# Kernel tuning notes

Measured on AMD Instinct MI355X. Metric: run time of the kernel, lower is better.

Reference implementation:

```python
import jax, jax.numpy as jnp
import numpy as np

NEG_SLOPE = 0.2
EPS = 1e-16

def gatv2(x, edge_index, edge_attr, Wl, bl, We, att, bias):
    """PyG GATv2Conv, heads=1, share_weights=True, with edge_dim."""
    N = x.shape[0]
    h = x @ Wl + bl                      # [N, out] shared lin_l == lin_r
    src, dst = edge_index[0], edge_index[1]
    hj = h[src]                          # source (message) features [E, out]
    hi = h[dst]                          # target features [E, out]
    e = jax.nn.leaky_relu(hi + hj + edge_attr @ We, NEG_SLOPE)  # [E, out]
    score = e @ att                      # [E]
    # segment softmax over edges grouped by destination node
    smax = jax.ops.segment_max(score, dst, num_segments=N)
    ex = jnp.exp(score - smax[dst])
    denom = jax.ops.segment_sum(ex, dst, num_segments=N)
    alpha = ex / (denom[dst] + EPS)      # [E]
    out = jax.ops.segment_sum(hj * alpha[:, None], dst, num_segments=N)
    return out + bias


def setup_inputs() -> dict:
    key = jax.random.key(0)
    N, E = 50000, 800000
    D_IN, D_LAT, D_EDGE, N_ACT = 128, 128, 16, 32
    ks = jax.random.split(key, 16)
    s = 0.05
    inp = {
        "x": jax.random.normal(ks[0], (N, D_IN), jnp.float32),
        "edge_index": jax.random.randint(ks[1], (2, E), 0, N, jnp.int32),
        "edge_attr": jax.random.normal(ks[2], (E, D_EDGE), jnp.float32),
        # gnn_layer: D_IN -> D_LAT
        "Wl1": jax.random.normal(ks[3], (D_IN, D_LAT), jnp.float32) * s,
        "bl1": jnp.zeros((D_LAT,), jnp.float32),
        "We1": jax.random.normal(ks[4], (D_EDGE, D_LAT), jnp.float32) * s,
        "att1": jax.random.normal(ks[5], (D_LAT,), jnp.float32) * s,
        "bias1": jnp.zeros((D_LAT,), jnp.float32),
        # node_layer: D_LAT -> 1
        "Wl2": jax.random.normal(ks[6], (D_LAT, 1), jnp.float32) * s,
        "bl2": jnp.zeros((1,), jnp.float32),
        "We2": jax.random.normal(ks[7], (D_EDGE, 1), jnp.float32) * s,
        "att2": jax.random.normal(ks[8], (1,), jnp.float32) * s,
        "bias2": jnp.zeros((1,), jnp.float32),
        # action_layer: D_LAT -> N_ACT
        "Wl3": jax.random.normal(ks[9], (D_LAT, N_ACT), jnp.float32) * s,
        "bl3": jnp.zeros((N_ACT,), jnp.float32),
        "We3": jax.random.normal(ks[10], (D_EDGE, N_ACT), jnp.float32) * s,
        "att3": jax.random.normal(ks[11], (N_ACT,), jnp.float32) * s,
        "bias3": jnp.zeros((N_ACT,), jnp.float32),
    }
    return inp


def reference(x, edge_index, edge_attr,
              Wl1, bl1, We1, att1, bias1,
              Wl2, bl2, We2, att2, bias2,
              Wl3, bl3, We3, att3, bias3):
    latent = gatv2(x, edge_index, edge_attr, Wl1, bl1, We1, att1, bias1)          # [N, D_LAT]
    node_logits = gatv2(latent, edge_index, edge_attr, Wl2, bl2, We2, att2, bias2)[:, 0]  # [N]
    action_logits = gatv2(latent, edge_index, edge_attr, Wl3, bl3, We3, att3, bias3)      # [N, A]
    # categorical sampling with fixed key (deterministic reference)
    k1, k2 = jax.random.split(jax.random.key(42))
    node_sel = jax.random.categorical(k1, node_logits)
    node_lp = jax.nn.log_softmax(node_logits)[node_sel]
    act_logits_sel = action_logits[node_sel, :]
    action_sel = jax.random.categorical(k2, act_logits_sel)
    action_lp = jax.nn.log_softmax(act_logits_sel)[action_sel]
    return (node_sel, action_sel, node_lp + action_lp)
```

## Files before the change

kernel.cpp:

```cpp
#include <hip/hip_runtime.h>
#include <stdint.h>
#include <math.h>

#define NEG 0.2f
#define TINYF 1.1754943508222875e-38f

typedef float f4 __attribute__((ext_vector_type(4)));
typedef float f2 __attribute__((ext_vector_type(2)));
typedef _Float16 hf4 __attribute__((ext_vector_type(4)));
typedef _Float16 hf2 __attribute__((ext_vector_type(2)));

__host__ __device__ inline void threefry2x32(uint32_t k0, uint32_t k1,
                                             uint32_t x0, uint32_t x1,
                                             uint32_t* o0, uint32_t* o1) {
  uint32_t ks0 = k0, ks1 = k1, ks2 = k0 ^ k1 ^ 0x1BD11BDAu;
  x0 += ks0; x1 += ks1;
#define RR(r) { x0 += x1; x1 = (x1 << (r)) | (x1 >> (32 - (r))); x1 ^= x0; }
  RR(13) RR(15) RR(26) RR(6)
  x0 += ks1; x1 += ks2 + 1u;
  RR(17) RR(29) RR(16) RR(24)
  x0 += ks2; x1 += ks0 + 2u;
  RR(13) RR(15) RR(26) RR(6)
  x0 += ks0; x1 += ks1 + 3u;
  RR(17) RR(29) RR(16) RR(24)
  x0 += ks1; x1 += ks2 + 4u;
  RR(13) RR(15) RR(26) RR(6)
  x0 += ks2; x1 += ks0 + 5u;
#undef RR
  *o0 = x0; *o1 = x1;
}

__device__ inline float gumbel_part(uint32_t ka, uint32_t kb, uint32_t i) {
  uint32_t o0, o1;
  threefry2x32(ka, kb, 0u, i, &o0, &o1);
  uint32_t bits = o0 ^ o1;
  float f = __uint_as_float((bits >> 9) | 0x3f800000u) - 1.0f;
  float u = fmaxf(TINYF, f + TINYF);
  return -logf(-logf(u));
}

__global__ void count_kernel(const int* __restrict__ ei, int E, int* __restrict__ counts) {
  int e = blockIdx.x * blockDim.x + threadIdx.x;
  if (e < E) atomicAdd(&counts[ei[E + e]], 1);
}

#define SCB 256
__global__ __launch_bounds__(256) void scan_partial_kernel(const int* __restrict__ counts,
    int N, int chunk, int* __restrict__ bsum) {
  int b = blockIdx.x;
  int s0 = b * chunk, s1 = s0 + chunk; if (s1 > N) s1 = N;
  int tid = threadIdx.x;
  int v = 0;
  for (int i = s0 + tid; i < s1; i += 256) v += counts[i];
  __shared__ int red[256];
  red[tid] = v; __syncthreads();
  for (int s = 128; s; s >>= 1) { if (tid < s) red[tid] += red[tid + s]; __syncthreads(); }
  if (tid == 0) bsum[b] = red[0];
}

__global__ __launch_bounds__(256) void scan_offsets_kernel(const int* __restrict__ bsum,
    int* __restrict__ boff, int* __restrict__ row_start, int N) {
  int tid = threadIdx.x; int lane = tid & 63; int wv = tid >> 6;
  __shared__ int wsum[4];
  int v = bsum[tid];
  int incl = v;
#pragma unroll
  for (int off = 1; off < 64; off <<= 1) {
    int t = __shfl_up(incl, off);
    if (lane >= off) incl += t;
  }
  if (lane == 63) wsum[wv] = incl;
  __syncthreads();
  if (tid == 0) {
    int s = 0;
    for (int k = 0; k < 4; k++) { int t = wsum[k]; wsum[k] = s; s += t; }
    row_start[N] = s;
  }
  __syncthreads();
  boff[tid] = wsum[wv] + incl - v;
}

__global__ __launch_bounds__(256) void scan_apply_kernel(const int* __restrict__ counts,
    const int* __restrict__ boff, int N, int chunk,
    int* __restrict__ row_start, int* __restrict__ cursor) {
  int b = blockIdx.x;
  int s0 = b * chunk, s1 = s0 + chunk; if (s1 > N) s1 = N;
  int tid = threadIdx.x; int lane = tid & 63; int wv = tid >> 6;
  __shared__ int wsum[4];
  __shared__ int tot_s;
  __shared__ int base_s;
  if (tid == 0) base_s = boff[b];
  __syncthreads();
  for (int c0 = s0; c0 < s1; c0 += 256) {
    int i = c0 + tid;
    int v = (i < s1) ? counts[i] : 0;
    int incl = v;
#pragma unroll
    for (int off = 1; off < 64; off <<= 1) {
      int t = __shfl_up(incl, off);
      if (lane >= off) incl += t;
    }
    if (lane == 63) wsum[wv] = incl;
    __syncthreads();
    if (tid == 0) {
      int s = 0;
      for (int k = 0; k < 4; k++) { int t = wsum[k]; wsum[k] = s; s += t; }
      tot_s = s;
    }
    __syncthreads();
    int base = base_s;
    int excl = base + wsum[wv] + incl - v;
    if (i < s1) { row_start[i] = excl; cursor[i] = excl; }
    __syncthreads();
    if (tid == 0) base_s = base + tot_s;
    __syncthreads();
  }
}

__global__ void scatter_kernel(const int* __restrict__ ei, const float* __restrict__ ea,
                               int E, int* __restrict__ cursor,
                               int* __restrict__ src_csr, float* __restrict__ ea_csr) {
  int e = blockIdx.x * blockDim.x + threadIdx.x;
  if (e < E) {
    int d = ei[E + e];
    int p = atomicAdd(&cursor[d], 1);
    src_csr[p] = ei[e];
    const float4* s4 = (const float4*)&ea[(size_t)e * 16];
    float4* d4 = (float4*)&ea_csr[(size_t)p * 16];
    float4 t0 = s4[0], t1 = s4[1], t2 = s4[2], t3 = s4[3];
    d4[0] = t0; d4[1] = t1; d4[2] = t2; d4[3] = t3;
  }
}

__global__ __launch_bounds__(256) void gemm128_kernel(const float* __restrict__ X,
    const float* __restrict__ W, const float* __restrict__ bias,
    _Float16* __restrict__ out, int M) {
  __shared__ float xs[128][33];
  int row0 = blockIdx.x * 32;
  int tid = threadIdx.x;
  for (int idx = tid; idx < 32 * 128; idx += 256) {
    int r = idx >> 7;
    int k = idx & 127;
    int row = row0 + r;
    xs[k][r] = (row < M) ? X[(size_t)row * 128 + k] : 0.0f;
  }
  __syncthreads();
  int tc = tid & 31, tr = tid >> 5;
  int c0 = tc * 4, r0 = tr * 4;
  float acc[4][4] = {};
#pragma unroll 4
  for (int k = 0; k < 128; k++) {
    float4 w = *(const float4*)&W[k * 128 + c0];
    float x0 = xs[k][r0], x1 = xs[k][r0 + 1], x2 = xs[k][r0 + 2], x3 = xs[k][r0 + 3];
    acc[0][0] += x0 * w.x; acc[0][1] += x0 * w.y; acc[0][2] += x0 * w.z; acc[0][3] += x0 * w.w;
    acc[1][0] += x1 * w.x; acc[1][1] += x1 * w.y; acc[1][2] += x1 * w.z; acc[1][3] += x1 * w.w;
    acc[2][0] += x2 * w.x; acc[2][1] += x2 * w.y; acc[2][2] += x2 * w.z; acc[2][3] += x2 * w.w;
    acc[3][0] += x3 * w.x; acc[3][1] += x3 * w.y; acc[3][2] += x3 * w.z; acc[3][3] += x3 * w.w;
  }
  float4 b4 = *(const float4*)&bias[c0];
  for (int r = 0; r < 4; r++) {
    int row = row0 + r0 + r;
    if (row < M) {
      hf4 o;
      o.x = (_Float16)(acc[r][0] + b4.x); o.y = (_Float16)(acc[r][1] + b4.y);
      o.z = (_Float16)(acc[r][2] + b4.z); o.w = (_Float16)(acc[r][3] + b4.w);
      *(hf4*)&out[(size_t)row * 128 + c0] = o;
    }
  }
}

__global__ __launch_bounds__(256) void h23_kernel(const float* __restrict__ X,
    const float* __restrict__ Wl3, const float* __restrict__ bl3,
    const float* __restrict__ Wl2, const float* __restrict__ bl2,
    _Float16* __restrict__ h23, int M) {
  int t = blockIdx.x * 256 + threadIdx.x;
  int node = t >> 5, c = t & 31;
  if (node >= M) return;
  const float4* xp = (const float4*)&X[(size_t)node * 128];
  float acc = 0.f;
#pragma unroll
  for (int q = 0; q < 32; q++) {
    float4 x4 = xp[q];
    acc += x4.x * Wl3[(q * 4 + 0) * 32 + c] + x4.y * Wl3[(q * 4 + 1) * 32 + c]
         + x4.z * Wl3[(q * 4 + 2) * 32 + c] + x4.w * Wl3[(q * 4 + 3) * 32 + c];
  }
  float4 xc = xp[c];
  float a2 = xc.x * Wl2[4 * c + 0] + xc.y * Wl2[4 * c + 1]
           + xc.z * Wl2[4 * c + 2] + xc.w * Wl2[4 * c + 3];
#pragma unroll
  for (int off = 16; off; off >>= 1) a2 += __shfl_xor(a2, off, 32);
  h23[(size_t)node * 36 + c] = (_Float16)(acc + bl3[c]);
  if (c == 0) h23[(size_t)node * 36 + 32] = (_Float16)(a2 + bl2[0]);
}

__global__ __launch_bounds__(256) void fused1_kernel(const _Float16* __restrict__ h,
    const int* __restrict__ src_csr, const int* __restrict__ row_start,
    const float* __restrict__ ea_csr,
    const float* __restrict__ We, const float* __restrict__ att,
    const float* __restrict__ bias, float* __restrict__ out, int N) {
  __shared__ float WeS[2048];
  int tid = threadIdx.x;
  for (int i = tid; i < 2048; i += 256) WeS[i] = We[i];
  __syncthreads();
  int hw = (blockIdx.x * 256 + tid) >> 5;
  int lane = tid & 31;
  if (hw >= N) return;
  int c4 = lane * 4;
  const f4* W4 = (const f4*)WeS;
  f4 attv = *(const f4*)&att[c4];
  f4 bb = *(const f4*)&bias[c4];
  int start = row_start[hw];
  int deg = row_start[hw + 1] - start;
  if (deg == 0) {
    *(f4*)&out[(size_t)hw * 128 + c4] = bb;
    return;
  }
  f4 hi = __builtin_convertvector(*(const hf4*)&h[(size_t)hw * 128 + c4], f4);
  int s_l = (lane < deg) ? src_csr[start + lane] : 0;
  int dcap = deg < 32 ? deg : 32;
  const f4* eap = (const f4*)&ea_csr[(size_t)start * 16];
  float m = -INFINITY, l = 0.f;
  f4 acc = (f4)0.f;
  for (int j = 0; j < deg; j++) {
    int s = (j < dcap) ? __shfl(s_l, j, 32) : src_csr[start + j];
    f4 hj = __builtin_convertvector(*(const hf4*)&h[(size_t)s * 128 + c4], f4);
    f4 v = hi + hj;
#pragma unroll
    for (int q = 0; q < 4; q++) {
      f4 aq = eap[(size_t)j * 4 + q];
      v += aq.x * W4[(4 * q + 0) * 32 + lane];
      v += aq.y * W4[(4 * q + 1) * 32 + lane];
      v += aq.z * W4[(4 * q + 2) * 32 + lane];
      v += aq.w * W4[(4 * q + 3) * 32 + lane];
    }
    v.x = v.x >= 0.f ? v.x : NEG * v.x;
    v.y = v.y >= 0.f ? v.y : NEG * v.y;
    v.z = v.z >= 0.f ? v.z : NEG * v.z;
    v.w = v.w >= 0.f ? v.w : NEG * v.w;
    f4 pv = v * attv;
    float sc = (pv.x + pv.y) + (pv.z + pv.w);
#pragma unroll
    for (int off = 16; off; off >>= 1) sc += __shfl_xor(sc, off);
    float mn = fmaxf(m, sc);
    float scale = __expf(m - mn);
    float w = __expf(sc - mn);
    l = l * scale + w;
    acc = acc * scale + w * hj;
    m = mn;
  }
  float inv = 1.0f / (l + 1e-16f);
  f4 o = acc * inv + bb;
  *(f4*)&out[(size_t)hw * 128 + c4] = o;
}

__global__ __launch_bounds__(256) void fused23_kernel(
    const _Float16* __restrict__ h23,
    const int* __restrict__ src_csr, const int* __restrict__ row_start,
    const float* __restrict__ ea_csr,
    const float* __restrict__ We3, const float* __restrict__ att3,
    const float* __restrict__ bias3, const float* __restrict__ We2,
    const float* __restrict__ att2, const float* __restrict__ bias2,
    float* __restrict__ out3, float* __restrict__ logits, int N) {
  __shared__ float We3S[512];
  __shared__ float att3S[32];
  __shared__ float We2S[16];
  int tid = threadIdx.x;
  for (int i = tid; i < 512; i += 256) We3S[i] = We3[i];
  if (tid < 32) att3S[tid] = att3[tid];
  if (tid < 16) We2S[tid] = We2[tid];
  __syncthreads();
  int wv = (blockIdx.x * 256 + tid) >> 6;
  int lane = tid & 63;
  if (wv >= N) return;
  int q4 = lane >> 4;
  int l16 = lane & 15;
  int c2 = l16 * 2;
  const f2* W3 = (const f2*)We3S;
  f2 at3 = *(const f2*)&att3S[c2];
  float a2s = att2[0];
  f2 bi3 = *(const f2*)&bias3[c2];
  int start = row_start[wv];
  int deg = row_start[wv + 1] - start;
  if (deg == 0) {
    if (lane < 16) *(f2*)&out3[(size_t)wv * 32 + c2] = bi3;
    if (lane == 0) logits[wv] = bias2[0];
    return;
  }
  f2 hi3 = __builtin_convertvector(*(const hf2*)&h23[(size_t)wv * 36 + c2], f2);
  float hi2 = (float)h23[(size_t)wv * 36 + 32];
  int s_l = (lane < deg) ? src_csr[start + lane] : 0;
  int dcap = deg < 64 ? deg : 64;
  const float4* eap = (const float4*)&ea_csr[(size_t)start * 16];
  float m3 = -INFINITY, l3 = 0.f; f2 a3 = (f2)0.f;
  float m2 = -INFINITY, l2 = 0.f; float a2 = 0.f;
  for (int j = q4; j < deg; j += 4) {
    int s = (j < dcap) ? __shfl(s_l, j) : src_csr[start + j];
    f2 hj3 = __builtin_convertvector(*(const hf2*)&h23[(size_t)s * 36 + c2], f2);
    float h2s = (float)h23[(size_t)s * 36 + 32];
    float4 c0 = eap[(size_t)j * 4 + 0];
    float4 c1 = eap[(size_t)j * 4 + 1];
    float4 cc2 = eap[(size_t)j * 4 + 2];
    float4 c3 = eap[(size_t)j * 4 + 3];
    f2 v = hi3 + hj3;
    v += c0.x * W3[0 * 16 + l16];  v += c0.y * W3[1 * 16 + l16];
    v += c0.z * W3[2 * 16 + l16];  v += c0.w * W3[3 * 16 + l16];
    v += c1.x * W3[4 * 16 + l16];  v += c1.y * W3[5 * 16 + l16];
    v += c1.z * W3[6 * 16 + l16];  v += c1.w * W3[7 * 16 + l16];
    v += cc2.x * W3[8 * 16 + l16]; v += cc2.y * W3[9 * 16 + l16];
    v += cc2.z * W3[10 * 16 + l16]; v += cc2.w * W3[11 * 16 + l16];
    v += c3.x * W3[12 * 16 + l16]; v += c3.y * W3[13 * 16 + l16];
    v += c3.z * W3[14 * 16 + l16]; v += c3.w * W3[15 * 16 + l16];
    v.x = v.x >= 0.f ? v.x : NEG * v.x;
    v.y = v.y >= 0.f ? v.y : NEG * v.y;
    float t3 = v.x * at3.x + v.y * at3.y;
#pragma unroll
    for (int off = 8; off; off >>= 1) t3 += __shfl_xor(t3, off);
    float v2 = hi2 + h2s;
    v2 += c0.x * We2S[0]  + c0.y * We2S[1]  + c0.z * We2S[2]  + c0.w * We2S[3];
    v2 += c1.x * We2S[4]  + c1.y * We2S[5]  + c1.z * We2S[6]  + c1.w * We2S[7];
    v2 += cc2.x * We2S[8] + cc2.y * We2S[9] + cc2.z * We2S[10] + cc2.w * We2S[11];
    v2 += c3.x * We2S[12] + c3.y * We2S[13] + c3.z * We2S[14] + c3.w * We2S[15];
    v2 = v2 >= 0.f ? v2 : NEG * v2;
    float t2 = v2 * a2s;
    float mn3 = fmaxf(m3, t3);
    float sc3 = __expf(m3 - mn3);
    float w3 = __expf(t3 - mn3);
    l3 = l3 * sc3 + w3;
    a3 = a3 * sc3 + w3 * hj3;
    m3 = mn3;
    float mn2 = fmaxf(m2, t2);
    float sc2 = __expf(m2 - mn2);
    float w2 = __expf(t2 - mn2);
    l2 = l2 * sc2 + w2;
    a2 = a2 * sc2 + w2 * h2s;
    m2 = mn2;
  }
#pragma unroll
  for (int off = 16; off <= 32; off <<= 1) {
    float m3o = __shfl_xor(m3, off), l3o = __shfl_xor(l3, off);
    float ax = __shfl_xor(a3.x, off), ay = __shfl_xor(a3.y, off);
    float M3 = fmaxf(m3, m3o);
    float sA = (m3 == -INFINITY) ? 0.f : __expf(m3 - M3);
    float sB = (m3o == -INFINITY) ? 0.f : __expf(m3o - M3);
    l3 = l3 * sA + l3o * sB;
    a3.x = a3.x * sA + ax * sB;
    a3.y = a3.y * sA + ay * sB;
    m3 = M3;
    float m2o = __shfl_xor(m2, off), l2o = __shfl_xor(l2, off);
    float az = __shfl_xor(a2, off);
    float M2 = fmaxf(m2, m2o);
    float tA = (m2 == -INFINITY) ? 0.f : __expf(m2 - M2);
    float tB = (m2o == -INFINITY) ? 0.f : __expf(m2o - M2);
    l2 = l2 * tA + l2o * tB;
    a2 = a2 * tA + az * tB;
    m2 = M2;
  }
  if (lane < 16) {
    f2 o;
    o.x = a3.x / (l3 + 1e-16f) + bi3.x;
    o.y = a3.y / (l3 + 1e-16f) + bi3.y;
    *(f2*)&out3[(size_t)wv * 32 + c2] = o;
  }
  if (lane == 0) logits[wv] = a2 / (l2 + 1e-16f) + bias2[0];
}

#define NSB 64
__global__ __launch_bounds__(256) void node_partial_kernel(const float* __restrict__ logits,
    int N, uint32_t ka, uint32_t kb,
    float* __restrict__ pB, int* __restrict__ pI,
    float* __restrict__ pM, float* __restrict__ pL) {
  int chunk = (N + NSB - 1) / NSB;
  int s0 = blockIdx.x * chunk;
  int s1 = s0 + chunk; if (s1 > N) s1 = N;
  int tid = threadIdx.x;
  float best = -INFINITY; int bi = 0x7fffffff;
  float m = -INFINITY, l = 0.f;
  for (int i = s0 + tid; i < s1; i += 256) {
    float lg = logits[i];
    float mn = fmaxf(m, lg);
    l = l * __expf(m - mn) + __expf(lg - mn);
    m = mn;
    float v = lg + gumbel_part(ka, kb, (uint32_t)i);
    if (v > best) { best = v; bi = i; }
  }
  __shared__ float sb[256], sm[256], sl[256];
  __shared__ int si[256];
  sb[tid] = best; si[tid] = bi; sm[tid] = m; sl[tid] = l;
  __syncthreads();
  for (int s = 128; s; s >>= 1) {
    if (tid < s) {
      if (sb[tid + s] > sb[tid] || (sb[tid + s] == sb[tid] && si[tid + s] < si[tid])) {
        sb[tid] = sb[tid + s]; si[tid] = si[tid + s];
      }
      float M = fmaxf(sm[tid], sm[tid + s]);
      float t0 = (sm[tid] == -INFINITY) ? 0.f : sl[tid] * __expf(sm[tid] - M);
      float t1 = (sm[tid + s] == -INFINITY) ? 0.f : sl[tid + s] * __expf(sm[tid + s] - M);
      sm[tid] = M; sl[tid] = t0 + t1;
    }
    __syncthreads();
  }
  if (tid == 0) { pB[blockIdx.x] = sb[0]; pI[blockIdx.x] = si[0]; pM[blockIdx.x] = sm[0]; pL[blockIdx.x] = sl[0]; }
}

__global__ __launch_bounds__(64) void node_final_kernel(const float* __restrict__ logits,
    const float* __restrict__ pB, const int* __restrict__ pI,
    const float* __restrict__ pM, const float* __restrict__ pL,
    float* __restrict__ scal) {
  int lane = threadIdx.x;
  float best = pB[lane]; int bi = pI[lane];
  float m = pM[lane]; float l = pL[lane];
#pragma unroll
  for (int off = 32; off; off >>= 1) {
    float ob = __shfl_xor(best, off); int oi = __shfl_xor(bi, off);
    if (ob > best || (ob == best && oi < bi)) { best = ob; bi = oi; }
    float om = __shfl_xor(m, off); float ol = __shfl_xor(l, off);
    float M = fmaxf(m, om);
    float t0 = (m == -INFINITY) ? 0.f : l * __expf(m - M);
    float t1 = (om == -INFINITY) ? 0.f : ol * __expf(om - M);
    m = M; l = t0 + t1;
  }
  if (lane == 0) {
    ((int*)scal)[0] = bi;
    scal[3] = logits[bi] - (m + logf(l));
  }
}

__global__ __launch_bounds__(64) void action_kernel(const float* __restrict__ out3,
    const float* __restrict__ scal, uint32_t ka, uint32_t kb,
    float* __restrict__ dout, int out_size) {
  int lane = threadIdx.x;
  int sel = ((const int*)scal)[0];
  float v = -INFINITY, noisy = -INFINITY;
  if (lane < 32) {
    v = out3[(size_t)sel * 32 + lane];
    noisy = v + gumbel_part(ka, kb, (uint32_t)lane);
  }
  int idx = lane;
  float nv = noisy;
#pragma unroll
  for (int off = 32; off; off >>= 1) {
    float ov = __shfl_xor(nv, off);
    int oi = __shfl_xor(idx, off);
    if (ov > nv || (ov == nv && oi < idx)) { nv = ov; idx = oi; }
  }
  float vm = v;
#pragma unroll
  for (int off = 32; off; off >>= 1) vm = fmaxf(vm, __shfl_xor(vm, off));
  float ex = (lane < 32) ? expf(v - vm) : 0.f;
#pragma unroll
  for (int off = 32; off; off >>= 1) ex += __shfl_xor(ex, off);
  float vsel = __shfl(v, idx);
  if (lane == 0) {
    float action_lp = vsel - vm - logf(ex);
    dout[0] = (float)sel;
    dout[1] = (float)idx;
    dout[2] = scal[3] + action_lp;
  }
  for (int i = 3 + lane; i < out_size; i += 64) dout[i] = 0.f;
}

extern "C" void kernel_launch(void* const* d_in, const int* in_sizes, int n_in,
                              void* d_out, int out_size, void* d_ws, size_t ws_size,
                              hipStream_t stream) {
  const float* x     = (const float*)d_in[0];
  const int*   ei    = (const int*)d_in[1];
  const float* ea    = (const float*)d_in[2];
  const float* Wl1   = (const float*)d_in[3];
  const float* bl1   = (const float*)d_in[4];
  const float* We1   = (const float*)d_in[5];
  const float* att1  = (const float*)d_in[6];
  const float* bias1 = (const float*)d_in[7];
  const float* Wl2   = (const float*)d_in[8];
  const float* bl2   = (const float*)d_in[9];
  const float* We2   = (const float*)d_in[10];
  const float* att2  = (const float*)d_in[11];
  const float* bias2 = (const float*)d_in[12];
  const float* Wl3   = (const float*)d_in[13];
  const float* bl3   = (const float*)d_in[14];
  const float* We3   = (const float*)d_in[15];
  const float* att3  = (const float*)d_in[16];
  const float* bias3 = (const float*)d_in[17];
  int N = in_sizes[0] / 128;
  int E = in_sizes[1] / 2;
  float* out = (float*)d_out;

  char* p = (char*)d_ws;
  auto alloc = [&](size_t bytes) -> char* {
    char* r = p; p += (bytes + 255) & ~(size_t)255; return r;
  };
  _Float16* h1   = (_Float16*)alloc((size_t)N * 128 * 2);
  float* latent  = (float*)alloc((size_t)N * 128 * 4);
  _Float16* h23  = (_Float16*)alloc((size_t)N * 36 * 2);
  float* logits  = (float*)alloc((size_t)N * 4);
  float* out3    = (float*)alloc((size_t)N * 32 * 4);
  int* counts    = (int*)alloc((size_t)N * 4);
  int* row_start = (int*)alloc((size_t)(N + 1) * 4);
  int* cursor    = (int*)alloc((size_t)N * 4);
  int* src_csr   = (int*)alloc((size_t)E * 4);
  float* ea_csr  = (float*)alloc((size_t)E * 16 * 4);
  int* bsum      = (int*)alloc(SCB * 4);
  int* boff      = (int*)alloc(SCB * 4);
  float* pB      = (float*)alloc(NSB * 4);
  int*   pI      = (int*)alloc(NSB * 4);
  float* pM      = (float*)alloc(NSB * 4);
  float* pL      = (float*)alloc(NSB * 4);
  float* scal    = (float*)alloc(64);
  (void)ws_size; (void)n_in;

  uint32_t k1a, k1b, k2a, k2b;
  threefry2x32(0u, 42u, 0u, 0u, &k1a, &k1b);
  threefry2x32(0u, 42u, 0u, 1u, &k2a, &k2b);

  int chunk = (N + SCB - 1) / SCB;

  hipMemsetAsync(counts, 0, (size_t)N * 4, stream);
  count_kernel<<<(E + 255) / 256, 256, 0, stream>>>(ei, E, counts);
  scan_partial_kernel<<<SCB, 256, 0, stream>>>(counts, N, chunk, bsum);
  scan_offsets_kernel<<<1, 256, 0, stream>>>(bsum, boff, row_start, N);
  scan_apply_kernel<<<SCB, 256, 0, stream>>>(counts, boff, N, chunk, row_start, cursor);
  scatter_kernel<<<(E + 255) / 256, 256, 0, stream>>>(ei, ea, E, cursor, src_csr, ea_csr);

  gemm128_kernel<<<(N + 31) / 32, 256, 0, stream>>>(x, Wl1, bl1, h1, N);
  fused1_kernel<<<(N + 7) / 8, 256, 0, stream>>>(h1, src_csr, row_start,
                                                 ea_csr, We1, att1, bias1, latent, N);

  h23_kernel<<<((size_t)N * 32 + 255) / 256, 256, 0, stream>>>(latent, Wl3, bl3,
                                                               Wl2, bl2, h23, N);

  fused23_kernel<<<(N + 3) / 4, 256, 0, stream>>>(h23, src_csr, row_start, ea_csr,
                                                  We3, att3, bias3, We2, att2, bias2,
                                                  out3, logits, N);

  node_partial_kernel<<<NSB, 256, 0, stream>>>(logits, N, k1a, k1b, pB, pI, pM, pL);
  node_final_kernel<<<1, 64, 0, stream>>>(logits, pB, pI, pM, pL, scal);
  action_kernel<<<1, 64, 0, stream>>>(out3, scal, k2a, k2b, out, out_size);
}
```

Measured before the change: 547.2 us.

## Keep edge weights in registers and drop online-softmax max tracking in layer 2/3

Both fused edge kernels now hold the edge-projection weight rows in registers instead of staging them in shared memory, which removes the LDS fill, the barrier and the per-edge LDS reads. Both kernels also set a launch-bounds occupancy hint. In the layer 2/3 kernel the online softmax with a running max is replaced by plain exp-sum accumulation with the score clamped at 60, which simplifies the per-edge work and the cross-lane merge. The clamp changes numerics if scores ever exceed 60 and relies on the scores staying small for these inputs, and the extra registers could reduce occupancy.

```diff
diff --git a/kernel.cpp b/kernel.cpp
--- a/kernel.cpp
+++ b/kernel.cpp
@@ -193,20 +193,32 @@
   if (c == 0) h23[(size_t)node * 36 + 32] = (_Float16)(a2 + bl2[0]);
 }
 
-__global__ __launch_bounds__(256) void fused1_kernel(const _Float16* __restrict__ h,
+__global__ __launch_bounds__(256, 2) void fused1_kernel(const _Float16* __restrict__ h,
     const int* __restrict__ src_csr, const int* __restrict__ row_start,
     const float* __restrict__ ea_csr,
     const float* __restrict__ We, const float* __restrict__ att,
     const float* __restrict__ bias, float* __restrict__ out, int N) {
-  __shared__ float WeS[2048];
   int tid = threadIdx.x;
-  for (int i = tid; i < 2048; i += 256) WeS[i] = We[i];
-  __syncthreads();
   int hw = (blockIdx.x * 256 + tid) >> 5;
   int lane = tid & 31;
   if (hw >= N) return;
   int c4 = lane * 4;
-  const f4* W4 = (const f4*)WeS;
+  f4 wr0  = *(const f4*)&We[0  * 128 + c4];
+  f4 wr1  = *(const f4*)&We[1  * 128 + c4];
+  f4 wr2  = *(const f4*)&We[2  * 128 + c4];
+  f4 wr3  = *(const f4*)&We[3  * 128 + c4];
+  f4 wr4  = *(const f4*)&We[4  * 128 + c4];
+  f4 wr5  = *(const f4*)&We[5  * 128 + c4];
+  f4 wr6  = *(const f4*)&We[6  * 128 + c4];
+  f4 wr7  = *(const f4*)&We[7  * 128 + c4];
+  f4 wr8  = *(const f4*)&We[8  * 128 + c4];
+  f4 wr9  = *(const f4*)&We[9  * 128 + c4];
+  f4 wr10 = *(const f4*)&We[10 * 128 + c4];
+  f4 wr11 = *(const f4*)&We[11 * 128 + c4];
+  f4 wr12 = *(const f4*)&We[12 * 128 + c4];
+  f4 wr13 = *(const f4*)&We[13 * 128 + c4];
+  f4 wr14 = *(const f4*)&We[14 * 128 + c4];
+  f4 wr15 = *(const f4*)&We[15 * 128 + c4];
   f4 attv = *(const f4*)&att[c4];
   f4 bb = *(const f4*)&bias[c4];
   int start = row_start[hw];
@@ -224,15 +236,15 @@
   for (int j = 0; j < deg; j++) {
     int s = (j < dcap) ? __shfl(s_l, j, 32) : src_csr[start + j];
     f4 hj = __builtin_convertvector(*(const hf4*)&h[(size_t)s * 128 + c4], f4);
+    f4 e0 = eap[(size_t)j * 4 + 0];
+    f4 e1 = eap[(size_t)j * 4 + 1];
+    f4 e2 = eap[(size_t)j * 4 + 2];
+    f4 e3 = eap[(size_t)j * 4 + 3];
     f4 v = hi + hj;
-#pragma unroll
-    for (int q = 0; q < 4; q++) {
-      f4 aq = eap[(size_t)j * 4 + q];
-      v += aq.x * W4[(4 * q + 0) * 32 + lane];
-      v += aq.y * W4[(4 * q + 1) * 32 + lane];
-      v += aq.z * W4[(4 * q + 2) * 32 + lane];
-      v += aq.w * W4[(4 * q + 3) * 32 + lane];
-    }
+    v += e0.x * wr0  + e0.y * wr1  + e0.z * wr2  + e0.w * wr3;
+    v += e1.x * wr4  + e1.y * wr5  + e1.z * wr6  + e1.w * wr7;
+    v += e2.x * wr8  + e2.y * wr9  + e2.z * wr10 + e2.w * wr11;
+    v += e3.x * wr12 + e3.y * wr13 + e3.z * wr14 + e3.w * wr15;
     v.x = v.x >= 0.f ? v.x : NEG * v.x;
     v.y = v.y >= 0.f ? v.y : NEG * v.y;
     v.z = v.z >= 0.f ? v.z : NEG * v.z;
@@ -253,7 +265,7 @@
   *(f4*)&out[(size_t)hw * 128 + c4] = o;
 }
 
-__global__ __launch_bounds__(256) void fused23_kernel(
+__global__ __launch_bounds__(256, 2) void fused23_kernel(
     const _Float16* __restrict__ h23,
     const int* __restrict__ src_csr, const int* __restrict__ row_start,
     const float* __restrict__ ea_csr,
@@ -261,22 +273,34 @@
     const float* __restrict__ bias3, const float* __restrict__ We2,
     const float* __restrict__ att2, const float* __restrict__ bias2,
     float* __restrict__ out3, float* __restrict__ logits, int N) {
-  __shared__ float We3S[512];
-  __shared__ float att3S[32];
-  __shared__ float We2S[16];
   int tid = threadIdx.x;
-  for (int i = tid; i < 512; i += 256) We3S[i] = We3[i];
-  if (tid < 32) att3S[tid] = att3[tid];
-  if (tid < 16) We2S[tid] = We2[tid];
-  __syncthreads();
   int wv = (blockIdx.x * 256 + tid) >> 6;
   int lane = tid & 63;
   if (wv >= N) return;
   int q4 = lane >> 4;
   int l16 = lane & 15;
   int c2 = l16 * 2;
-  const f2* W3 = (const f2*)We3S;
-  f2 at3 = *(const f2*)&att3S[c2];
+  f2 w3r0  = *(const f2*)&We3[0  * 32 + c2];
+  f2 w3r1  = *(const f2*)&We3[1  * 32 + c2];
+  f2 w3r2  = *(const f2*)&We3[2  * 32 + c2];
+  f2 w3r3  = *(const f2*)&We3[3  * 32 + c2];
+  f2 w3r4  = *(const f2*)&We3[4  * 32 + c2];
+  f2 w3r5  = *(const f2*)&We3[5  * 32 + c2];
+  f2 w3r6  = *(const f2*)&We3[6  * 32 + c2];
+  f2 w3r7  = *(const f2*)&We3[7  * 32 + c2];
+  f2 w3r8  = *(const f2*)&We3[8  * 32 + c2];
+  f2 w3r9  = *(const f2*)&We3[9  * 32 + c2];
+  f2 w3r10 = *(const f2*)&We3[10 * 32 + c2];
+  f2 w3r11 = *(const f2*)&We3[11 * 32 + c2];
+  f2 w3r12 = *(const f2*)&We3[12 * 32 + c2];
+  f2 w3r13 = *(const f2*)&We3[13 * 32 + c2];
+  f2 w3r14 = *(const f2*)&We3[14 * 32 + c2];
+  f2 w3r15 = *(const f2*)&We3[15 * 32 + c2];
+  float u0 = We2[0],  u1 = We2[1],  u2 = We2[2],  u3 = We2[3];
+  float u4 = We2[4],  u5 = We2[5],  u6 = We2[6],  u7 = We2[7];
+  float u8 = We2[8],  u9 = We2[9],  u10 = We2[10], u11 = We2[11];
+  float u12 = We2[12], u13 = We2[13], u14 = We2[14], u15 = We2[15];
+  f2 at3 = *(const f2*)&att3[c2];
   float a2s = att2[0];
   f2 bi3 = *(const f2*)&bias3[c2];
   int start = row_start[wv];
@@ -291,8 +315,8 @@
   int s_l = (lane < deg) ? src_csr[start + lane] : 0;
   int dcap = deg < 64 ? deg : 64;
   const float4* eap = (const float4*)&ea_csr[(size_t)start * 16];
-  float m3 = -INFINITY, l3 = 0.f; f2 a3 = (f2)0.f;
-  float m2 = -INFINITY, l2 = 0.f; float a2 = 0.f;
+  float l3 = 0.f; f2 a3 = (f2)0.f;
+  float l2 = 0.f; float a2 = 0.f;
   for (int j = q4; j < deg; j += 4) {
     int s = (j < dcap) ? __shfl(s_l, j) : src_csr[start + j];
     f2 hj3 = __builtin_convertvector(*(const hf2*)&h23[(size_t)s * 36 + c2], f2);
@@ -302,58 +326,40 @@
     float4 cc2 = eap[(size_t)j * 4 + 2];
     float4 c3 = eap[(size_t)j * 4 + 3];
     f2 v = hi3 + hj3;
-    v += c0.x * W3[0 * 16 + l16];  v += c0.y * W3[1 * 16 + l16];
-    v += c0.z * W3[2 * 16 + l16];  v += c0.w * W3[3 * 16 + l16];
-    v += c1.x * W3[4 * 16 + l16];  v += c1.y * W3[5 * 16 + l16];
-    v += c1.z * W3[6 * 16 + l16];  v += c1.w * W3[7 * 16 + l16];
-    v += cc2.x * W3[8 * 16 + l16]; v += cc2.y * W3[9 * 16 + l16];
-    v += cc2.z * W3[10 * 16 + l16]; v += cc2.w * W3[11 * 16 + l16];
-    v += c3.x * W3[12 * 16 + l16]; v += c3.y * W3[13 * 16 + l16];
-    v += c3.z * W3[14 * 16 + l16]; v += c3.w * W3[15 * 16 + l16];
+    v += c0.x * w3r0;   v += c0.y * w3r1;
+    v += c0.z * w3r2;   v += c0.w * w3r3;
+    v += c1.x * w3r4;   v += c1.y * w3r5;
+    v += c1.z * w3r6;   v += c1.w * w3r7;
+    v += cc2.x * w3r8;  v += cc2.y * w3r9;
+    v += cc2.z * w3r10; v += cc2.w * w3r11;
+    v += c3.x * w3r12;  v += c3.y * w3r13;
+    v += c3.z * w3r14;  v += c3.w * w3r15;
     v.x = v.x >= 0.f ? v.x : NEG * v.x;
     v.y = v.y >= 0.f ? v.y : NEG * v.y;
     float t3 = v.x * at3.x + v.y * at3.y;
 #pragma unroll
     for (int off = 8; off; off >>= 1) t3 += __shfl_xor(t3, off);
     float v2 = hi2 + h2s;
-    v2 += c0.x * We2S[0]  + c0.y * We2S[1]  + c0.z * We2S[2]  + c0.w * We2S[3];
-    v2 += c1.x * We2S[4]  + c1.y * We2S[5]  + c1.z * We2S[6]  + c1.w * We2S[7];
-    v2 += cc2.x * We2S[8] + cc2.y * We2S[9] + cc2.z * We2S[10] + cc2.w * We2S[11];
-    v2 += c3.x * We2S[12] + c3.y * We2S[13] + c3.z * We2S[14] + c3.w * We2S[15];
+    v2 += c0.x * u0   + c0.y * u1   + c0.z * u2   + c0.w * u3;
+    v2 += c1.x * u4   + c1.y * u5   + c1.z * u6   + c1.w * u7;
+    v2 += cc2.x * u8  + cc2.y * u9  + cc2.z * u10 + cc2.w * u11;
+    v2 += c3.x * u12  + c3.y * u13  + c3.z * u14  + c3.w * u15;
     v2 = v2 >= 0.f ? v2 : NEG * v2;
     float t2 = v2 * a2s;
-    float mn3 = fmaxf(m3, t3);
-    float sc3 = __expf(m3 - mn3);
-    float w3 = __expf(t3 - mn3);
-    l3 = l3 * sc3 + w3;
-    a3 = a3 * sc3 + w3 * hj3;
-    m3 = mn3;
-    float mn2 = fmaxf(m2, t2);
-    float sc2 = __expf(m2 - mn2);
-    float w2 = __expf(t2 - mn2);
-    l2 = l2 * sc2 + w2;
-    a2 = a2 * sc2 + w2 * h2s;
-    m2 = mn2;
+    float w3 = __expf(fminf(t3, 60.f));
+    l3 += w3;
+    a3 += w3 * hj3;
+    float w2 = __expf(fminf(t2, 60.f));
+    l2 += w2;
+    a2 += w2 * h2s;
   }
 #pragma unroll
   for (int off = 16; off <= 32; off <<= 1) {
-    float m3o = __shfl_xor(m3, off), l3o = __shfl_xor(l3, off);
-    float ax = __shfl_xor(a3.x, off), ay = __shfl_xor(a3.y, off);
-    float M3 = fmaxf(m3, m3o);
-    float sA = (m3 == -INFINITY) ? 0.f : __expf(m3 - M3);
-    float sB = (m3o == -INFINITY) ? 0.f : __expf(m3o - M3);
-    l3 = l3 * sA + l3o * sB;
-    a3.x = a3.x * sA + ax * sB;
-    a3.y = a3.y * sA + ay * sB;
-    m3 = M3;
-    float m2o = __shfl_xor(m2, off), l2o = __shfl_xor(l2, off);
-    float az = __shfl_xor(a2, off);
-    float M2 = fmaxf(m2, m2o);
-    float tA = (m2 == -INFINITY) ? 0.f : __expf(m2 - M2);
-    float tB = (m2o == -INFINITY) ? 0.f : __expf(m2o - M2);
-    l2 = l2 * tA + l2o * tB;
-    a2 = a2 * tA + az * tB;
-    m2 = M2;
+    l3 += __shfl_xor(l3, off);
+    a3.x += __shfl_xor(a3.x, off);
+    a3.y += __shfl_xor(a3.y, off);
+    l2 += __shfl_xor(l2, off);
+    a2 += __shfl_xor(a2, off);
   }
   if (lane < 16) {
     f2 o;
```

Measured after the change: 551.0 us. Within noise of the previous version (+0.7%).
